# Optimization experiments

Hardware: AMD Instinct MI355X
Metric: run time of the kernel (lower is better)

## Reference

```python
import jax, jax.numpy as jnp
import numpy as np

N_USERS = 100000
N_ITEMS = 50000
DIM = 64
N_LAYERS = 3          # lightGCN_n_layers
SEM_LAYERS = 2        # semantic_layers
SEM_WEIGHT = 0.5      # semantic_weight
UI_NNZ = 5000000
II_NNZ = 1600000
N_NODES = N_USERS + N_ITEMS


def setup_inputs() -> dict:
    key = jax.random.key(0)
    ks = jax.random.split(key, 8)
    user_emb = 0.1 * jax.random.normal(ks[0], (N_USERS, DIM), dtype=jnp.float32)
    item_emb = 0.1 * jax.random.normal(ks[1], (N_ITEMS, DIM), dtype=jnp.float32)
    # normalized adjacency values are small positive (D^-1/2 A D^-1/2)
    ui_val = 0.01 * jax.random.uniform(ks[2], (UI_NNZ,), dtype=jnp.float32)
    ii_val = 0.01 * jax.random.uniform(ks[3], (II_NNZ,), dtype=jnp.float32)
    ui_src = jax.random.randint(ks[4], (UI_NNZ,), 0, N_NODES, dtype=jnp.int32)
    ui_dst = jax.random.randint(ks[5], (UI_NNZ,), 0, N_NODES, dtype=jnp.int32)
    ii_src = jax.random.randint(ks[6], (II_NNZ,), 0, N_ITEMS, dtype=jnp.int32)
    ii_dst = jax.random.randint(ks[7], (II_NNZ,), 0, N_ITEMS, dtype=jnp.int32)
    return {"user_emb": user_emb, "item_emb": item_emb,
            "ui_val": ui_val, "ii_val": ii_val,
            "ui_src": ui_src, "ui_dst": ui_dst,
            "ii_src": ii_src, "ii_dst": ii_dst}


def _spmm(src, dst, val, x, n_rows):
    """out[dst] += val * x[src]  (COO sparse matmul, gather-scale-scatter)."""
    return jax.ops.segment_sum(val[:, None] * x[src], dst, num_segments=n_rows)


def reference(user_emb, item_emb, ui_val, ii_val, ui_src, ui_dst, ii_src, ii_dst):
    # ---- CF propagation on User-Item bipartite graph ----
    all_emb = jnp.concatenate([user_emb, item_emb], axis=0)  # [N_NODES, D]
    acc = all_emb
    cur = all_emb
    for _ in range(N_LAYERS):
        cur = _spmm(ui_src, ui_dst, ui_val, cur, N_NODES)
        acc = acc + cur
    light_out_ui = acc / (N_LAYERS + 1)  # mean over stacked layers
    users_emb_ui = light_out_ui[:N_USERS]
    items_emb_ui = light_out_ui[N_USERS:]

    # ---- Semantic propagation on Item-Item graph ----
    acc_ii = item_emb
    cur_ii = item_emb
    for _ in range(SEM_LAYERS):
        cur_ii = _spmm(ii_src, ii_dst, ii_val, cur_ii, N_ITEMS)
        acc_ii = acc_ii + cur_ii
    items_emb_sem = acc_ii / (SEM_LAYERS + 1)

    # ---- Fusion (as in getUsersRating / bpr_loss) ----
    all_items = (1.0 - SEM_WEIGHT) * items_emb_ui + SEM_WEIGHT * items_emb_sem
    return jnp.concatenate([users_emb_ui, all_items], axis=0)  # [N_NODES, D]
```

## Files before the change

kernel.cpp:

```cpp
#include <hip/hip_runtime.h>
#include <hip/hip_fp16.h>

#define N_USERS 100000
#define N_ITEMS 50000
#define N_NODES 150000

#define SROWS 512
#define SSHIFT 9
#define NB_UI 293
#define NB_II 98
#define UI_CAP 18432
#define II_CAP 17408
#define CHUNK 4096
#define DEQ (0.01f / 16383.0f)

__device__ __forceinline__ void fma_mix_lo(float& acc, float w, unsigned xh) {
    asm("v_fma_mix_f32 %0, %1, %2, %0 op_sel:[0,0,0] op_sel_hi:[0,1,0]"
        : "+v"(acc) : "v"(w), "v"(xh));
}
__device__ __forceinline__ void fma_mix_hi(float& acc, float w, unsigned xh) {
    asm("v_fma_mix_f32 %0, %1, %2, %0 op_sel:[0,1,0] op_sel_hi:[0,1,0]"
        : "+v"(acc) : "v"(w), "v"(xh));
}

__device__ inline uint2 pack4h(float4 v) {
    uint2 h;
    h.x = (unsigned)__half_as_ushort(__float2half(v.x)) |
          ((unsigned)__half_as_ushort(__float2half(v.y)) << 16);
    h.y = (unsigned)__half_as_ushort(__float2half(v.z)) |
          ((unsigned)__half_as_ushort(__float2half(v.w)) << 16);
    return h;
}

__global__ void init_concat(const float4* __restrict__ user_emb,
                            const float4* __restrict__ item_emb,
                            uint2* __restrict__ curH,
                            float4* __restrict__ acc,
                            uint2* __restrict__ itemH) {
    int i = blockIdx.x * blockDim.x + threadIdx.x;
    const int n = N_NODES * 16;
    if (i >= n) return;
    bool is_item = (i >= N_USERS * 16);
    float4 v = is_item ? item_emb[i - N_USERS * 16] : user_emb[i];
    acc[i] = v;
    uint2 h = pack4h(v);
    curH[i] = h;
    if (is_item) itemH[i - N_USERS * 16] = h;
}

__global__ void count_dual(const int* __restrict__ uiD, const int* __restrict__ iiD,
                           int* __restrict__ cntU, int* __restrict__ cntI,
                           int ui_nnz, int ii_nnz, int gU) {
    __shared__ int h[512];
    const bool isU = (int)blockIdx.x < gU;
    const int* __restrict__ dst = isU ? uiD : iiD;
    int* __restrict__ cnts = isU ? cntU : cntI;
    const int nnz = isU ? ui_nnz : ii_nnz;
    const int nbuckets = isU ? NB_UI : NB_II;
    const int chunk = isU ? blockIdx.x : blockIdx.x - gU;

    for (int i = threadIdx.x; i < 512; i += blockDim.x) h[i] = 0;
    __syncthreads();
    int c0 = chunk * CHUNK;
    int c1 = min(c0 + CHUNK, nnz);
    for (int e = c0 + threadIdx.x; e < c1; e += blockDim.x)
        atomicAdd(&h[dst[e] >> SSHIFT], 1);
    __syncthreads();
    for (int i = threadIdx.x; i < nbuckets; i += blockDim.x)
        cnts[(size_t)chunk * nbuckets + i] = h[i];
}

__global__ void scan_dual(int* __restrict__ cntU, int* __restrict__ cntI,
                          int* __restrict__ frontU, int* __restrict__ frontI,
                          int gU, int gI) {
    __shared__ int s[512];
    const bool isU = (int)blockIdx.x < NB_UI;
    const int b = isU ? blockIdx.x : blockIdx.x - NB_UI;
    int* __restrict__ C = (isU ? cntU : cntI) + b;
    int* __restrict__ frontier = isU ? frontU : frontI;
    const int stride = isU ? NB_UI : NB_II;
    const int n = isU ? gU : gI;
    const int tid = threadIdx.x;

    int carry = 0;
    for (int t0 = 0; t0 < n; t0 += 512) {
        int c = t0 + tid;
        int v = (c < n) ? C[(size_t)c * stride] : 0;
        s[tid] = v;
        __syncthreads();
        for (int off2 = 1; off2 < 512; off2 <<= 1) {
            int u = (tid >= off2) ? s[tid - off2] : 0;
            __syncthreads();
            s[tid] += u;
            __syncthreads();
        }
        if (c < n) C[(size_t)c * stride] = carry + s[tid] - v;
        carry += s[511];
        __syncthreads();
    }
    if (tid == 0) frontier[b] = carry;
}

__global__ void __launch_bounds__(512) scatter_dual(
                             const int* __restrict__ uiS, const int* __restrict__ uiD,
                             const float* __restrict__ uiV,
                             const int* __restrict__ iiS, const int* __restrict__ iiD,
                             const float* __restrict__ iiV,
                             const int* __restrict__ cntU, const int* __restrict__ cntI,
                             const int* __restrict__ frontU, const int* __restrict__ frontI,
                             uint2* __restrict__ outU, uint2* __restrict__ outI,
                             int ui_nnz, int ii_nnz, int gU, int gI) {
    __shared__ int s[512];
    __shared__ int pre2[512];
    __shared__ int fill[512];
    __shared__ uint2 stage[CHUNK];
    const bool isU = (int)blockIdx.x < gU;
    const int* __restrict__ src = isU ? uiS : iiS;
    const int* __restrict__ dst = isU ? uiD : iiD;
    const float* __restrict__ val = isU ? uiV : iiV;
    const int* __restrict__ cnts = isU ? cntU : cntI;
    const int* __restrict__ front = isU ? frontU : frontI;
    uint2* __restrict__ out = isU ? outU : outI;
    const int nnz = isU ? ui_nnz : ii_nnz;
    const int nb = isU ? NB_UI : NB_II;
    const int cap = isU ? UI_CAP : II_CAP;
    const int gcnt = isU ? gU : gI;
    const int chunk = isU ? blockIdx.x : blockIdx.x - gU;
    const int tid = threadIdx.x;

    int cnt_i = 0, pre_i = 0;
    if (tid < nb) {
        pre_i = cnts[(size_t)chunk * nb + tid];
        int nx = (chunk + 1 < gcnt) ? cnts[(size_t)(chunk + 1) * nb + tid] : front[tid];
        cnt_i = nx - pre_i;
    }
    s[tid] = cnt_i;
    __syncthreads();
    for (int off2 = 1; off2 < 512; off2 <<= 1) {
        int u = (tid >= off2) ? s[tid - off2] : 0;
        __syncthreads();
        s[tid] += u;
        __syncthreads();
    }
    int lo_excl = s[tid] - cnt_i;
    if (tid < nb) {
        pre2[tid] = tid * cap + pre_i - lo_excl;
        fill[tid] = lo_excl;
    }
    __syncthreads();

    int c0 = chunk * CHUNK;
    int c1 = min(c0 + CHUNK, nnz);
    for (int e = c0 + tid; e < c1; e += 512) {
        int d = dst[e];
        int b = d >> SSHIFT;
        unsigned q = __float2uint_rn(val[e] * 1638300.0f);
        q = min(q, 16383u);
        uint2 r;
        r.x = (unsigned)src[e] | ((unsigned)b << 18);
        r.y = ((unsigned)(d & (SROWS - 1)) << 14) | q;
        int p = atomicAdd(&fill[b], 1);
        stage[p] = r;
    }
    __syncthreads();

    int n = c1 - c0;
    for (int p = tid; p < n; p += 512) {
        uint2 r = stage[p];
        int b = r.x >> 18;
        r.x &= 0x3FFFFu;
        int addr = pre2[b] + p;
        int lim = (b + 1) * cap;
        if (addr >= lim) addr = lim - 1;
        out[addr] = r;
    }
}

__global__ void sort_dual(const int* __restrict__ bcU, const int* __restrict__ bcI,
                          const uint2* __restrict__ inU, const uint2* __restrict__ inI,
                          unsigned* __restrict__ outU, unsigned* __restrict__ outI,
                          int* __restrict__ reU, int* __restrict__ reI) {
    __shared__ int cnt[SROWS];
    __shared__ int scn[SROWS];
    __shared__ int fill[SROWS];
    const bool isU = (int)blockIdx.x < NB_UI;
    const int b = isU ? blockIdx.x : blockIdx.x - NB_UI;
    const int* __restrict__ bcnt = isU ? bcU : bcI;
    const uint2* __restrict__ in = isU ? inU : inI;
    unsigned* __restrict__ out = isU ? outU : outI;
    int* __restrict__ rowend = isU ? reU : reI;
    const int n_rows = isU ? N_NODES : N_ITEMS;
    const int cap = isU ? UI_CAP : II_CAP;

    int tid = threadIdx.x;
    int n = min(bcnt[b], cap);
    int s = b * cap;
    cnt[tid] = 0;
    __syncthreads();
    for (int j = tid; j < n; j += 512)
        atomicAdd(&cnt[in[s + j].y >> 14], 1);
    __syncthreads();
    scn[tid] = cnt[tid];
    __syncthreads();
    for (int off2 = 1; off2 < SROWS; off2 <<= 1) {
        int v = (tid >= off2) ? scn[tid - off2] : 0;
        __syncthreads();
        scn[tid] += v;
        __syncthreads();
    }
    fill[tid] = scn[tid] - cnt[tid];
    int gr = b * SROWS + tid;
    if (gr < n_rows) rowend[gr] = s + scn[tid];
    __syncthreads();
    for (int j = tid; j < n; j += 512) {
        uint2 r = in[s + j];
        int row = r.y >> 14;
        int pos = s + atomicAdd(&fill[row], 1);
        out[pos] = (r.x << 14) | (r.y & 16383u);
    }
}

#define PQ_EDGE(S, OFF) { e##S##0 = edges[eb + (OFF)]; e##S##1 = edges[eb + (OFF) + 1]; }
#define PQ_GATH(S) { \
    g##S##0 = *(const uint2*)(xb + (((e##S##0 >> 14) << 7) + co)); \
    g##S##1 = *(const uint2*)(xb + (((e##S##1 >> 14) << 7) + co)); \
    w##S##0 = (float)(e##S##0 & 16383u) * DEQ; \
    w##S##1 = (float)(e##S##1 & 16383u) * DEQ; }
#define PQ_CONS(S) { \
    fma_mix_lo(a0, w##S##0, (g##S##0).x); fma_mix_hi(a1, w##S##0, (g##S##0).x); \
    fma_mix_lo(a2, w##S##0, (g##S##0).y); fma_mix_hi(a3, w##S##0, (g##S##0).y); \
    fma_mix_lo(b0, w##S##1, (g##S##1).x); fma_mix_hi(b1, w##S##1, (g##S##1).x); \
    fma_mix_lo(b2, w##S##1, (g##S##1).y); fma_mix_hi(b3, w##S##1, (g##S##1).y); }

__device__ __forceinline__ float4 pull_quad(const int* __restrict__ rowend,
                                            const unsigned* __restrict__ edges,
                                            const __half* __restrict__ x,
                                            int row, int cap, int g, unsigned co) {
    int start = (row & (SROWS - 1)) ? rowend[row - 1] : (row >> SSHIFT) * cap;
    int end = rowend[row];
    float a0 = 0.f, a1 = 0.f, a2 = 0.f, a3 = 0.f;
    float b0 = 0.f, b1 = 0.f, b2 = 0.f, b3 = 0.f;
    const char* xb = (const char*)x;
    const int e0 = start + 2 * g;
    const int nfull = (end - start) >> 3;

    unsigned eA0, eA1, eB0, eB1, eC0, eC1, eD0, eD1;
    uint2 gA0, gA1, gB0, gB1, gC0, gC1, gD0, gD1;
    float wA0, wA1, wB0, wB1, wC0, wC1, wD0, wD1;

    int eb = e0;
    if (nfull > 0) PQ_EDGE(A, 0);
    if (nfull > 1) PQ_EDGE(B, 8);
    if (nfull > 2) PQ_EDGE(C, 16);
    if (nfull > 3) PQ_EDGE(D, 24);
    if (nfull > 0) PQ_GATH(A);
    if (nfull > 1) PQ_GATH(B);
    if (nfull > 2) PQ_GATH(C);

    int k = 0;
    for (; k + 8 <= nfull; k += 4, eb += 32) {
        PQ_EDGE(A, 32); PQ_GATH(D); PQ_CONS(A);
        PQ_EDGE(B, 40); PQ_GATH(A); PQ_CONS(B);
        PQ_EDGE(C, 48); PQ_GATH(B); PQ_CONS(C);
        PQ_EDGE(D, 56); PQ_GATH(C); PQ_CONS(D);
    }
    {
        int r = nfull - k;
        if (r > 0) { if (r > 3) PQ_GATH(D);                       PQ_CONS(A); }
        if (r > 1) { if (r > 4) { PQ_EDGE(A, 32); PQ_GATH(A); }   PQ_CONS(B); }
        if (r > 2) { if (r > 5) { PQ_EDGE(B, 40); PQ_GATH(B); }   PQ_CONS(C); }
        if (r > 3) { if (r > 6) { PQ_EDGE(C, 48); PQ_GATH(C); }   PQ_CONS(D); }
        if (r > 4) PQ_CONS(A);
        if (r > 5) PQ_CONS(B);
        if (r > 6) PQ_CONS(C);
    }
    int jt = start + 8 * nfull;
    if (jt < end) {
        int et = e0 + 8 * nfull;
        int last = end - 1;
        int i0 = min(et, last);
        int i1 = min(et + 1, last);
        unsigned r0 = edges[i0];
        unsigned r1 = edges[i1];
        uint2 u0 = *(const uint2*)(xb + (((r0 >> 14) << 7) + co));
        uint2 u1 = *(const uint2*)(xb + (((r1 >> 14) << 7) + co));
        float w0 = (et <= last) ? (float)(r0 & 16383u) * DEQ : 0.f;
        float w1 = (et + 1 <= last) ? (float)(r1 & 16383u) * DEQ : 0.f;
        fma_mix_lo(a0, w0, u0.x); fma_mix_hi(a1, w0, u0.x);
        fma_mix_lo(a2, w0, u0.y); fma_mix_hi(a3, w0, u0.y);
        fma_mix_lo(b0, w1, u1.x); fma_mix_hi(b1, w1, u1.x);
        fma_mix_lo(b2, w1, u1.y); fma_mix_hi(b3, w1, u1.y);
    }
    a0 += b0; a1 += b1; a2 += b2; a3 += b3;
    a0 += __shfl_xor(a0, 16); a1 += __shfl_xor(a1, 16);
    a2 += __shfl_xor(a2, 16); a3 += __shfl_xor(a3, 16);
    a0 += __shfl_xor(a0, 32); a1 += __shfl_xor(a1, 32);
    a2 += __shfl_xor(a2, 32); a3 += __shfl_xor(a3, 32);
    return make_float4(a0, a1, a2, a3);
}

template<int MODE>
__global__ void __launch_bounds__(256) spmm_pull(
                          const int* __restrict__ rowend,
                          const unsigned* __restrict__ edges,
                          const __half* __restrict__ x,
                          __half* __restrict__ y,
                          float* __restrict__ acc,
                          int n_rows, int cap) {
    int row = blockIdx.x * 4 + (threadIdx.x >> 6);
    if (row >= n_rows) return;
    const int lane = threadIdx.x & 63;
    const int g = lane >> 4;
    const int c4 = lane & 15;
    float4 A = pull_quad(rowend, edges, x, row, cap, g, (unsigned)c4 << 3);
    if (g != 0) return;
    size_t o4 = (size_t)row * 16 + c4;
    union { __half2 h[2]; uint2 u; } cv;
    cv.h[0] = __float22half2_rn(make_float2(A.x, A.y));
    cv.h[1] = __float22half2_rn(make_float2(A.z, A.w));
    ((uint2*)y)[o4] = cv.u;
    if (MODE == 0) {
        float4* A4 = (float4*)acc;
        float4 v = A4[o4];
        v.x += A.x; v.y += A.y; v.z += A.z; v.w += A.w;
        A4[o4] = v;
    }
}

__global__ void __launch_bounds__(256) spmm_l1_dual(
                          const int* __restrict__ reU, const unsigned* __restrict__ eU,
                          const __half* __restrict__ xU, __half* __restrict__ yU,
                          float* __restrict__ accU,
                          const int* __restrict__ reI, const unsigned* __restrict__ eI,
                          const __half* __restrict__ xI, __half* __restrict__ yI,
                          int nbU) {
    const int lane = threadIdx.x & 63;
    const int g = lane >> 4;
    const int c4 = lane & 15;
    const unsigned co = (unsigned)c4 << 3;
    if ((int)blockIdx.x < nbU) {
        int row = blockIdx.x * 4 + (threadIdx.x >> 6);
        if (row >= N_NODES) return;
        float4 A = pull_quad(reU, eU, xU, row, UI_CAP, g, co);
        if (g != 0) return;
        size_t o4 = (size_t)row * 16 + c4;
        union { __half2 h[2]; uint2 u; } cv;
        cv.h[0] = __float22half2_rn(make_float2(A.x, A.y));
        cv.h[1] = __float22half2_rn(make_float2(A.z, A.w));
        ((uint2*)yU)[o4] = cv.u;
        float4* A4 = (float4*)accU;
        float4 v = A4[o4];
        v.x += A.x; v.y += A.y; v.z += A.z; v.w += A.w;
        A4[o4] = v;
    } else {
        int row = (blockIdx.x - nbU) * 4 + (threadIdx.x >> 6);
        if (row >= N_ITEMS) return;
        float4 A = pull_quad(reI, eI, xI, row, II_CAP, g, co);
        if (g != 0) return;
        size_t o4 = (size_t)row * 16 + c4;
        union { __half2 h[2]; uint2 u; } cv;
        cv.h[0] = __float22half2_rn(make_float2(A.x, A.y));
        cv.h[1] = __float22half2_rn(make_float2(A.z, A.w));
        ((uint2*)yI)[o4] = cv.u;
    }
}

__global__ void __launch_bounds__(256) spmm_final(
                          const int* __restrict__ reU, const unsigned* __restrict__ eU,
                          const __half* __restrict__ xU,
                          const int* __restrict__ reI, const unsigned* __restrict__ eI,
                          const __half* __restrict__ xI,
                          const __half* __restrict__ itemH,
                          float* __restrict__ out) {
    int row = blockIdx.x * 4 + (threadIdx.x >> 6);
    if (row >= N_NODES) return;
    const int lane = threadIdx.x & 63;
    const int g = lane >> 4;
    const int c4 = lane & 15;
    const unsigned co = (unsigned)c4 << 3;
    float4 A = pull_quad(reU, eU, xU, row, UI_CAP, g, co);
    float4* O4 = (float4*)out;
    if (row < N_USERS) {
        if (g != 0) return;
        size_t o4 = (size_t)row * 16 + c4;
        float4 v = O4[o4];
        v.x = 0.25f * (v.x + A.x); v.y = 0.25f * (v.y + A.y);
        v.z = 0.25f * (v.z + A.z); v.w = 0.25f * (v.w + A.w);
        O4[o4] = v;
    } else {
        int r = row - N_USERS;
        float4 Bq = pull_quad(reI, eI, xI, r, II_CAP, g, co);
        if (g != 0) return;
        size_t o4 = (size_t)row * 16 + c4;
        size_t i4 = (size_t)r * 16 + c4;
        uint2 ih = ((const uint2*)itemH)[i4];
        uint2 z1 = ((const uint2*)xI)[i4];
        float2 ih0 = __half22float2(*(const __half2*)&ih.x);
        float2 ih1 = __half22float2(*(const __half2*)&ih.y);
        float2 z10 = __half22float2(*(const __half2*)&z1.x);
        float2 z11 = __half22float2(*(const __half2*)&z1.y);
        float4 v = O4[o4];
        v.x = 0.125f * (v.x + A.x) + (ih0.x + z10.x + Bq.x) * (1.0f / 6.0f);
        v.y = 0.125f * (v.y + A.y) + (ih0.y + z10.y + Bq.y) * (1.0f / 6.0f);
        v.z = 0.125f * (v.z + A.z) + (ih1.x + z11.x + Bq.z) * (1.0f / 6.0f);
        v.w = 0.125f * (v.w + A.w) + (ih1.y + z11.y + Bq.w) * (1.0f / 6.0f);
        O4[o4] = v;
    }
}

extern "C" void kernel_launch(void* const* d_in, const int* in_sizes, int n_in,
                              void* d_out, int out_size, void* d_ws, size_t ws_size,
                              hipStream_t stream) {
    const float* user_emb = (const float*)d_in[0];
    const float* item_emb = (const float*)d_in[1];
    const float* ui_val   = (const float*)d_in[2];
    const float* ii_val   = (const float*)d_in[3];
    const int*   ui_src   = (const int*)d_in[4];
    const int*   ui_dst   = (const int*)d_in[5];
    const int*   ii_src   = (const int*)d_in[6];
    const int*   ii_dst   = (const int*)d_in[7];
    float* out = (float*)d_out;

    const int ui_nnz = in_sizes[2];
    const int ii_nnz = in_sizes[3];

    char* base = (char*)d_ws;
    size_t off = 0;
    __half* curU  = (__half*)(base + off); off += (size_t)N_NODES * 64 * 2;
    __half* nxtU  = (__half*)(base + off); off += (size_t)N_NODES * 64 * 2;
    __half* itemH = (__half*)(base + off); off += (size_t)N_ITEMS * 64 * 2;
    uint2* tempU  = (uint2*)base;
    uint2* tempI  = (uint2*)d_out;
    int* cntU = (int*)((char*)d_out + 18ull * 1024 * 1024);
    int* cntI = (int*)((char*)d_out + 21ull * 1024 * 1024);
    unsigned* uiEdgeS = (unsigned*)(base + off); off += 4ull * NB_UI * UI_CAP;
    unsigned* iiEdgeS = (unsigned*)(base + off); off += 4ull * NB_II * II_CAP;
    __half* bufA  = (__half*)(base + off); off += (size_t)N_ITEMS * 64 * 2;
    int* frontU  = (int*)(base + off); off += 4ull * NB_UI;
    int* frontI  = (int*)(base + off); off += 4ull * NB_II;
    int* rowendU = (int*)(base + off); off += 4ull * N_NODES;
    int* rowendI = (int*)(base + off); off += 4ull * N_ITEMS;

    const int B = 256;
    const int gU = (ui_nnz + CHUNK - 1) / CHUNK;
    const int gI = (ii_nnz + CHUNK - 1) / CHUNK;

    count_dual<<<gU + gI, B, 0, stream>>>(ui_dst, ii_dst, cntU, cntI,
                                          ui_nnz, ii_nnz, gU);
    scan_dual<<<NB_UI + NB_II, 512, 0, stream>>>(cntU, cntI, frontU, frontI, gU, gI);
    scatter_dual<<<gU + gI, 512, 0, stream>>>(ui_src, ui_dst, ui_val,
                                              ii_src, ii_dst, ii_val,
                                              cntU, cntI, frontU, frontI,
                                              tempU, tempI,
                                              ui_nnz, ii_nnz, gU, gI);
    sort_dual<<<NB_UI + NB_II, SROWS, 0, stream>>>(frontU, frontI, tempU, tempI,
                                                   uiEdgeS, iiEdgeS, rowendU, rowendI);

    init_concat<<<(N_NODES * 16 + B - 1) / B, B, 0, stream>>>(
        (const float4*)user_emb, (const float4*)item_emb,
        (uint2*)curU, (float4*)out, (uint2*)itemH);

    const int nbU = (N_NODES + 3) / 4;
    const int nbI = (N_ITEMS + 3) / 4;
    spmm_l1_dual<<<nbU + nbI, B, 0, stream>>>(rowendU, uiEdgeS, curU, nxtU, out,
                                              rowendI, iiEdgeS, itemH, bufA, nbU);
    spmm_pull<0><<<nbU, B, 0, stream>>>(rowendU, uiEdgeS, nxtU, curU, out, N_NODES, UI_CAP);
    spmm_final<<<nbU, B, 0, stream>>>(rowendU, uiEdgeS, curU,
                                      rowendI, iiEdgeS, bufA, itemH, out);
}
```

Baseline: 599.2 us.

## Drop fp32 accumulator traffic and map two rows per wavefront in SpMM pulls

Removes the fp32 running accumulator that was written at init and read-modified-written after each layer. The final kernel now rebuilds the layer sum from the original fp32 embeddings plus the fp16 layer outputs (y1, y2), which cuts global memory traffic. Each wavefront now processes two rows with two edge groups of 16 lanes each, instead of one row with four groups, giving more row parallelism and one fewer shuffle-reduction stage. The trade-offs are that intermediate layer values now enter the sum at fp16 precision, and rows with many edges have less per-row parallelism.

```diff
diff --git a/kernel.cpp b/kernel.cpp
--- a/kernel.cpp
+++ b/kernel.cpp
@@ -31,18 +31,21 @@
           ((unsigned)__half_as_ushort(__float2half(v.w)) << 16);
     return h;
 }
+__device__ inline float4 h4_to_f4(uint2 u) {
+    float2 lo = __half22float2(*(const __half2*)&u.x);
+    float2 hi = __half22float2(*(const __half2*)&u.y);
+    return make_float4(lo.x, lo.y, hi.x, hi.y);
+}
 
 __global__ void init_concat(const float4* __restrict__ user_emb,
                             const float4* __restrict__ item_emb,
                             uint2* __restrict__ curH,
-                            float4* __restrict__ acc,
                             uint2* __restrict__ itemH) {
     int i = blockIdx.x * blockDim.x + threadIdx.x;
     const int n = N_NODES * 16;
     if (i >= n) return;
     bool is_item = (i >= N_USERS * 16);
     float4 v = is_item ? item_emb[i - N_USERS * 16] : user_emb[i];
-    acc[i] = v;
     uint2 h = pack4h(v);
     curH[i] = h;
     if (is_item) itemH[i - N_USERS * 16] = h;
@@ -232,17 +235,17 @@
     fma_mix_lo(b0, w##S##1, (g##S##1).x); fma_mix_hi(b1, w##S##1, (g##S##1).x); \
     fma_mix_lo(b2, w##S##1, (g##S##1).y); fma_mix_hi(b3, w##S##1, (g##S##1).y); }
 
-__device__ __forceinline__ float4 pull_quad(const int* __restrict__ rowend,
-                                            const unsigned* __restrict__ edges,
-                                            const __half* __restrict__ x,
-                                            int row, int cap, int g, unsigned co) {
+__device__ __forceinline__ float4 pull2(const int* __restrict__ rowend,
+                                        const unsigned* __restrict__ edges,
+                                        const __half* __restrict__ x,
+                                        int row, int cap, int g2, unsigned co) {
     int start = (row & (SROWS - 1)) ? rowend[row - 1] : (row >> SSHIFT) * cap;
     int end = rowend[row];
     float a0 = 0.f, a1 = 0.f, a2 = 0.f, a3 = 0.f;
     float b0 = 0.f, b1 = 0.f, b2 = 0.f, b3 = 0.f;
     const char* xb = (const char*)x;
-    const int e0 = start + 2 * g;
-    const int nfull = (end - start) >> 3;
+    const int e0 = start + 2 * g2;
+    const int nfull = (end - start) >> 2;
 
     unsigned eA0, eA1, eB0, eB1, eC0, eC1, eD0, eD1;
     uint2 gA0, gA1, gB0, gB1, gC0, gC1, gD0, gD1;
@@ -250,33 +253,33 @@
 
     int eb = e0;
     if (nfull > 0) PQ_EDGE(A, 0);
-    if (nfull > 1) PQ_EDGE(B, 8);
-    if (nfull > 2) PQ_EDGE(C, 16);
-    if (nfull > 3) PQ_EDGE(D, 24);
+    if (nfull > 1) PQ_EDGE(B, 4);
+    if (nfull > 2) PQ_EDGE(C, 8);
+    if (nfull > 3) PQ_EDGE(D, 12);
     if (nfull > 0) PQ_GATH(A);
     if (nfull > 1) PQ_GATH(B);
     if (nfull > 2) PQ_GATH(C);
 
     int k = 0;
-    for (; k + 8 <= nfull; k += 4, eb += 32) {
-        PQ_EDGE(A, 32); PQ_GATH(D); PQ_CONS(A);
-        PQ_EDGE(B, 40); PQ_GATH(A); PQ_CONS(B);
-        PQ_EDGE(C, 48); PQ_GATH(B); PQ_CONS(C);
-        PQ_EDGE(D, 56); PQ_GATH(C); PQ_CONS(D);
+    for (; k + 8 <= nfull; k += 4, eb += 16) {
+        PQ_EDGE(A, 16); PQ_GATH(D); PQ_CONS(A);
+        PQ_EDGE(B, 20); PQ_GATH(A); PQ_CONS(B);
+        PQ_EDGE(C, 24); PQ_GATH(B); PQ_CONS(C);
+        PQ_EDGE(D, 28); PQ_GATH(C); PQ_CONS(D);
     }
     {
         int r = nfull - k;
         if (r > 0) { if (r > 3) PQ_GATH(D);                       PQ_CONS(A); }
-        if (r > 1) { if (r > 4) { PQ_EDGE(A, 32); PQ_GATH(A); }   PQ_CONS(B); }
-        if (r > 2) { if (r > 5) { PQ_EDGE(B, 40); PQ_GATH(B); }   PQ_CONS(C); }
-        if (r > 3) { if (r > 6) { PQ_EDGE(C, 48); PQ_GATH(C); }   PQ_CONS(D); }
+        if (r > 1) { if (r > 4) { PQ_EDGE(A, 16); PQ_GATH(A); }   PQ_CONS(B); }
+        if (r > 2) { if (r > 5) { PQ_EDGE(B, 20); PQ_GATH(B); }   PQ_CONS(C); }
+        if (r > 3) { if (r > 6) { PQ_EDGE(C, 24); PQ_GATH(C); }   PQ_CONS(D); }
         if (r > 4) PQ_CONS(A);
         if (r > 5) PQ_CONS(B);
         if (r > 6) PQ_CONS(C);
     }
-    int jt = start + 8 * nfull;
+    int jt = start + 4 * nfull;
     if (jt < end) {
-        int et = e0 + 8 * nfull;
+        int et = e0 + 4 * nfull;
         int last = end - 1;
         int i0 = min(et, last);
         int i1 = min(et + 1, last);
@@ -294,116 +297,97 @@
     a0 += b0; a1 += b1; a2 += b2; a3 += b3;
     a0 += __shfl_xor(a0, 16); a1 += __shfl_xor(a1, 16);
     a2 += __shfl_xor(a2, 16); a3 += __shfl_xor(a3, 16);
-    a0 += __shfl_xor(a0, 32); a1 += __shfl_xor(a1, 32);
-    a2 += __shfl_xor(a2, 32); a3 += __shfl_xor(a3, 32);
     return make_float4(a0, a1, a2, a3);
 }
 
-template<int MODE>
-__global__ void __launch_bounds__(256) spmm_pull(
+__global__ void __launch_bounds__(256) spmm_y(
                           const int* __restrict__ rowend,
                           const unsigned* __restrict__ edges,
                           const __half* __restrict__ x,
                           __half* __restrict__ y,
-                          float* __restrict__ acc,
-                          int n_rows, int cap) {
-    int row = blockIdx.x * 4 + (threadIdx.x >> 6);
-    if (row >= n_rows) return;
+                          int cap) {
     const int lane = threadIdx.x & 63;
-    const int g = lane >> 4;
+    int row = blockIdx.x * 8 + (threadIdx.x >> 6) * 2 + (lane >> 5);
+    const int g2 = (lane >> 4) & 1;
     const int c4 = lane & 15;
-    float4 A = pull_quad(rowend, edges, x, row, cap, g, (unsigned)c4 << 3);
-    if (g != 0) return;
+    float4 A = pull2(rowend, edges, x, row, cap, g2, (unsigned)c4 << 3);
+    if (lane & 16) return;
     size_t o4 = (size_t)row * 16 + c4;
     union { __half2 h[2]; uint2 u; } cv;
     cv.h[0] = __float22half2_rn(make_float2(A.x, A.y));
     cv.h[1] = __float22half2_rn(make_float2(A.z, A.w));
     ((uint2*)y)[o4] = cv.u;
-    if (MODE == 0) {
-        float4* A4 = (float4*)acc;
-        float4 v = A4[o4];
-        v.x += A.x; v.y += A.y; v.z += A.z; v.w += A.w;
-        A4[o4] = v;
-    }
 }
 
 __global__ void __launch_bounds__(256) spmm_l1_dual(
                           const int* __restrict__ reU, const unsigned* __restrict__ eU,
                           const __half* __restrict__ xU, __half* __restrict__ yU,
-                          float* __restrict__ accU,
                           const int* __restrict__ reI, const unsigned* __restrict__ eI,
                           const __half* __restrict__ xI, __half* __restrict__ yI,
                           int nbU) {
+    const bool isU = (int)blockIdx.x < nbU;
+    const int* __restrict__ rowend = isU ? reU : reI;
+    const unsigned* __restrict__ edges = isU ? eU : eI;
+    const __half* __restrict__ x = isU ? xU : xI;
+    __half* __restrict__ y = isU ? yU : yI;
+    const int cap = isU ? UI_CAP : II_CAP;
+    const int blk = isU ? blockIdx.x : blockIdx.x - nbU;
     const int lane = threadIdx.x & 63;
-    const int g = lane >> 4;
+    int row = blk * 8 + (threadIdx.x >> 6) * 2 + (lane >> 5);
+    const int g2 = (lane >> 4) & 1;
     const int c4 = lane & 15;
-    const unsigned co = (unsigned)c4 << 3;
-    if ((int)blockIdx.x < nbU) {
-        int row = blockIdx.x * 4 + (threadIdx.x >> 6);
-        if (row >= N_NODES) return;
-        float4 A = pull_quad(reU, eU, xU, row, UI_CAP, g, co);
-        if (g != 0) return;
-        size_t o4 = (size_t)row * 16 + c4;
-        union { __half2 h[2]; uint2 u; } cv;
-        cv.h[0] = __float22half2_rn(make_float2(A.x, A.y));
-        cv.h[1] = __float22half2_rn(make_float2(A.z, A.w));
-        ((uint2*)yU)[o4] = cv.u;
-        float4* A4 = (float4*)accU;
-        float4 v = A4[o4];
-        v.x += A.x; v.y += A.y; v.z += A.z; v.w += A.w;
-        A4[o4] = v;
-    } else {
-        int row = (blockIdx.x - nbU) * 4 + (threadIdx.x >> 6);
-        if (row >= N_ITEMS) return;
-        float4 A = pull_quad(reI, eI, xI, row, II_CAP, g, co);
-        if (g != 0) return;
-        size_t o4 = (size_t)row * 16 + c4;
-        union { __half2 h[2]; uint2 u; } cv;
-        cv.h[0] = __float22half2_rn(make_float2(A.x, A.y));
-        cv.h[1] = __float22half2_rn(make_float2(A.z, A.w));
-        ((uint2*)yI)[o4] = cv.u;
-    }
+    float4 A = pull2(rowend, edges, x, row, cap, g2, (unsigned)c4 << 3);
+    if (lane & 16) return;
+    size_t o4 = (size_t)row * 16 + c4;
+    union { __half2 h[2]; uint2 u; } cv;
+    cv.h[0] = __float22half2_rn(make_float2(A.x, A.y));
+    cv.h[1] = __float22half2_rn(make_float2(A.z, A.w));
+    ((uint2*)y)[o4] = cv.u;
 }
 
 __global__ void __launch_bounds__(256) spmm_final(
                           const int* __restrict__ reU, const unsigned* __restrict__ eU,
                           const __half* __restrict__ xU,
+                          const __half* __restrict__ y1,
+                          const float4* __restrict__ uemb,
+                          const float4* __restrict__ iemb,
                           const int* __restrict__ reI, const unsigned* __restrict__ eI,
                           const __half* __restrict__ xI,
-                          const __half* __restrict__ itemH,
                           float* __restrict__ out) {
-    int row = blockIdx.x * 4 + (threadIdx.x >> 6);
-    if (row >= N_NODES) return;
     const int lane = threadIdx.x & 63;
-    const int g = lane >> 4;
+    int row = blockIdx.x * 8 + (threadIdx.x >> 6) * 2 + (lane >> 5);
+    const int g2 = (lane >> 4) & 1;
     const int c4 = lane & 15;
     const unsigned co = (unsigned)c4 << 3;
-    float4 A = pull_quad(reU, eU, xU, row, UI_CAP, g, co);
+    float4 A = pull2(reU, eU, xU, row, UI_CAP, g2, co);
     float4* O4 = (float4*)out;
     if (row < N_USERS) {
-        if (g != 0) return;
+        if (lane & 16) return;
         size_t o4 = (size_t)row * 16 + c4;
-        float4 v = O4[o4];
-        v.x = 0.25f * (v.x + A.x); v.y = 0.25f * (v.y + A.y);
-        v.z = 0.25f * (v.z + A.z); v.w = 0.25f * (v.w + A.w);
+        float4 e0 = uemb[o4];
+        float4 f1 = h4_to_f4(((const uint2*)y1)[o4]);
+        float4 f2 = h4_to_f4(((const uint2*)xU)[o4]);
+        float4 v;
+        v.x = 0.25f * (e0.x + f1.x + f2.x + A.x);
+        v.y = 0.25f * (e0.y + f1.y + f2.y + A.y);
+        v.z = 0.25f * (e0.z + f1.z + f2.z + A.z);
+        v.w = 0.25f * (e0.w + f1.w + f2.w + A.w);
         O4[o4] = v;
     } else {
         int r = row - N_USERS;
-        float4 Bq = pull_quad(reI, eI, xI, r, II_CAP, g, co);
-        if (g != 0) return;
+        float4 Bq = pull2(reI, eI, xI, r, II_CAP, g2, co);
+        if (lane & 16) return;
         size_t o4 = (size_t)row * 16 + c4;
         size_t i4 = (size_t)r * 16 + c4;
-        uint2 ih = ((const uint2*)itemH)[i4];
-        uint2 z1 = ((const uint2*)xI)[i4];
-        float2 ih0 = __half22float2(*(const __half2*)&ih.x);
-        float2 ih1 = __half22float2(*(const __half2*)&ih.y);
-        float2 z10 = __half22float2(*(const __half2*)&z1.x);
-        float2 z11 = __half22float2(*(const __half2*)&z1.y);
-        float4 v = O4[o4];
-        v.x = 0.125f * (v.x + A.x) + (ih0.x + z10.x + Bq.x) * (1.0f / 6.0f);
-        v.y = 0.125f * (v.y + A.y) + (ih0.y + z10.y + Bq.y) * (1.0f / 6.0f);
-        v.z = 0.125f * (v.z + A.z) + (ih1.x + z11.x + Bq.z) * (1.0f / 6.0f);
-        v.w = 0.125f * (v.w + A.w) + (ih1.y + z11.y + Bq.w) * (1.0f / 6.0f);
+        float4 e0 = iemb[i4];
+        float4 f1 = h4_to_f4(((const uint2*)y1)[o4]);
+        float4 f2 = h4_to_f4(((const uint2*)xU)[o4]);
+        float4 z1 = h4_to_f4(((const uint2*)xI)[i4]);
+        float4 v;
+        v.x = 0.125f * (e0.x + f1.x + f2.x + A.x) + (e0.x + z1.x + Bq.x) * (1.0f / 6.0f);
+        v.y = 0.125f * (e0.y + f1.y + f2.y + A.y) + (e0.y + z1.y + Bq.y) * (1.0f / 6.0f);
+        v.z = 0.125f * (e0.z + f1.z + f2.z + A.z) + (e0.z + z1.z + Bq.z) * (1.0f / 6.0f);
+        v.w = 0.125f * (e0.w + f1.w + f2.w + A.w) + (e0.w + z1.w + Bq.w) * (1.0f / 6.0f);
         O4[o4] = v;
     }
 }
@@ -458,13 +442,14 @@
 
     init_concat<<<(N_NODES * 16 + B - 1) / B, B, 0, stream>>>(
         (const float4*)user_emb, (const float4*)item_emb,
-        (uint2*)curU, (float4*)out, (uint2*)itemH);
-
-    const int nbU = (N_NODES + 3) / 4;
-    const int nbI = (N_ITEMS + 3) / 4;
-    spmm_l1_dual<<<nbU + nbI, B, 0, stream>>>(rowendU, uiEdgeS, curU, nxtU, out,
+        (uint2*)curU, (uint2*)itemH);
+
+    const int nbU = N_NODES / 8;
+    const int nbI = N_ITEMS / 8;
+    spmm_l1_dual<<<nbU + nbI, B, 0, stream>>>(rowendU, uiEdgeS, curU, nxtU,
                                               rowendI, iiEdgeS, itemH, bufA, nbU);
-    spmm_pull<0><<<nbU, B, 0, stream>>>(rowendU, uiEdgeS, nxtU, curU, out, N_NODES, UI_CAP);
-    spmm_final<<<nbU, B, 0, stream>>>(rowendU, uiEdgeS, curU,
-                                      rowendI, iiEdgeS, bufA, itemH, out);
-}
+    spmm_y<<<nbU, B, 0, stream>>>(rowendU, uiEdgeS, nxtU, curU, UI_CAP);
+    spmm_final<<<nbU, B, 0, stream>>>(rowendU, uiEdgeS, curU, nxtU,
+                                      (const float4*)user_emb, (const float4*)item_emb,
+                                      rowendI, iiEdgeS, bufA, out);
+}
```

Result: faster. 562.7 us (-6.1%).
